# Kernel tuning notes

Measured on AMD Instinct MI355X. Metric: run time of the kernel, lower is better.

The kernel has to match this reference:

```python
import jax, jax.numpy as jnp
import numpy as np

N = 100_000   # nodes
E = 1_600_000 # edges (avg degree 16)
D = 128       # dim == dim_out
NEG_SLOPE = 0.2  # PyG GATConv default


def setup_inputs() -> dict:
    key = jax.random.key(0)
    ks = jax.random.split(key, 11)
    s = 1.0 / np.sqrt(D)
    return {
        "x": jax.random.normal(ks[0], (N, D), jnp.float32),
        "edge_index": jax.random.randint(ks[1], (2, E), 0, N, jnp.int32),
        "W1": jax.random.normal(ks[2], (D, D), jnp.float32) * s,
        "a_src1": jax.random.normal(ks[3], (D,), jnp.float32) * s,
        "a_dst1": jax.random.normal(ks[4], (D,), jnp.float32) * s,
        "b1": jnp.zeros((D,), jnp.float32),
        "W2": jax.random.normal(ks[5], (D, D), jnp.float32) * s,
        "a_src2": jax.random.normal(ks[6], (D,), jnp.float32) * s,
        "a_dst2": jax.random.normal(ks[7], (D,), jnp.float32) * s,
        "b2": jnp.zeros((D,), jnp.float32),
    }


def gat_conv(x, W, a_src, a_dst, b, src, dst, n):
    # PyG GATConv, heads=1: message flows src (j) -> dst (i)
    h = x @ W                              # [n, d]
    al_src = h @ a_src                     # per-node src attention logit
    al_dst = h @ a_dst                     # per-node dst attention logit
    e = jax.nn.leaky_relu(al_src[src] + al_dst[dst], NEG_SLOPE)  # [E']
    # softmax over incoming edges of each destination node (segment softmax)
    m = jax.ops.segment_max(e, dst, num_segments=n)
    e = jnp.exp(e - m[dst])
    z = jax.ops.segment_sum(e, dst, num_segments=n)
    alpha = e / z[dst]                     # [E']
    out = jax.ops.segment_sum(h[src] * alpha[:, None], dst, num_segments=n)
    return out + b


def reference(x, edge_index, W1, a_src1, a_dst1, b1, W2, a_src2, a_dst2, b2):
    n = x.shape[0]
    loop = jnp.arange(n, dtype=edge_index.dtype)
    src = jnp.concatenate([edge_index[0], loop])  # add_self_loops=True
    dst = jnp.concatenate([edge_index[1], loop])
    h = gat_conv(x, W1, a_src1, a_dst1, b1, src, dst, n)
    # self_loops=True -> residual=False; dropout in eval mode = identity
    return gat_conv(h, W2, a_src2, a_dst2, b2, src, dst, n)
```

## Files before the change

### kernel.cpp

```cpp
#include <hip/hip_runtime.h>
#include <hip/hip_bf16.h>
#include <math.h>

#define D 128
#define LRELU_SLOPE 0.2f
#define BSH 9
#define BSZ 512
#define BCAP 10240
#define SC_CHUNK 16384

typedef __attribute__((ext_vector_type(8))) short bf16x8;
typedef __attribute__((ext_vector_type(4))) float f32x4;

__device__ __forceinline__ float lrelu(float x){ return x > 0.f ? x : LRELU_SLOPE * x; }

__device__ __forceinline__ unsigned short bf16_rn(float x){
  unsigned int u = __float_as_uint(x);
  return (unsigned short)((u + 0x7FFFu + ((u >> 16) & 1u)) >> 16);
}
__device__ __forceinline__ float bf16_lo_f(unsigned int u){ return __uint_as_float(u << 16); }
__device__ __forceinline__ float bf16_hi_f(unsigned int u){ return __uint_as_float(u & 0xFFFF0000u); }

__device__ __forceinline__ unsigned int enc_f(float f){
  unsigned int u = __float_as_uint(f);
  return (u & 0x80000000u) ? ~u : (u | 0x80000000u);
}
__device__ __forceinline__ float dec_f(unsigned int e){
  return __uint_as_float((e & 0x80000000u) ? (e & 0x7FFFFFFFu) : ~e);
}

__global__ __launch_bounds__(1024) void bucket_scatter_kernel(const int* __restrict__ src,
    const int* __restrict__ dst, int E, int* __restrict__ bcur,
    unsigned int* __restrict__ ebuf, int nbuck){
  __shared__ int h[256];
  __shared__ int cb[256];
  int t = threadIdx.x;
  int base = blockIdx.x * SC_CHUNK;
  int end = base + SC_CHUNK; if (end > E) end = E;
  if (t < 256) h[t] = 0;
  __syncthreads();
  for (int e = base + t; e < end; e += 1024)
    atomicAdd(&h[dst[e] >> BSH], 1);
  __syncthreads();
  if (t < nbuck){
    cb[t] = h[t] ? atomicAdd(&bcur[t], h[t]) : 0;
    h[t] = 0;
  }
  __syncthreads();
  for (int e = base + t; e < end; e += 1024){
    int d = dst[e];
    int b = d >> BSH;
    int lpos = atomicAdd(&h[b], 1);
    ebuf[cb[b] + lpos] = ((unsigned int)src[e] << BSH) | (unsigned int)(d & (BSZ-1));
  }
}

__global__ __launch_bounds__(256) void bucket_csr_kernel(const unsigned int* __restrict__ ebuf,
    const int* __restrict__ bcur, int2* __restrict__ rowrange, int* __restrict__ colb,
    int n, int nbuck){
  __shared__ int c[512];
  __shared__ int ps[256];
  int b = blockIdx.x;
  int t = threadIdx.x;
  int base = b * BCAP;
  int end  = bcur[b];
  c[t] = 0; c[t+256] = 0;
  __syncthreads();
  for (int i = base + t; i < end; i += 256)
    atomicAdd(&c[ebuf[i] & (BSZ-1)], 1);
  __syncthreads();
  int a0 = c[2*t], a1 = c[2*t+1];
  int pair = a0 + a1;
  ps[t] = pair;
  __syncthreads();
  #pragma unroll
  for (int d = 1; d < 256; d <<= 1){
    int add = (t >= d) ? ps[t-d] : 0;
    __syncthreads();
    ps[t] += add;
    __syncthreads();
  }
  int excl = ps[t] - pair;
  __syncthreads();
  int lo = b << BSH;
  int g0 = lo + 2*t, g1 = g0 + 1;
  if (g0 < n) rowrange[g0] = make_int2(base + excl,      base + excl + a0);
  if (g1 < n) rowrange[g1] = make_int2(base + excl + a0, base + excl + a0 + a1);
  c[2*t]   = excl;
  c[2*t+1] = excl + a0;
  __syncthreads();
  for (int i = base + t; i < end; i += 256){
    unsigned int p = ebuf[i];
    int dlo = p & (BSZ-1);
    int pos = base + atomicAdd(&c[dlo], 1);
    colb[pos] = (int)(p >> BSH);
  }
}

__global__ __launch_bounds__(256) void wsplit_kernel(const float* __restrict__ W1,
    const float* __restrict__ W2,
    unsigned short* __restrict__ Whf1, unsigned short* __restrict__ Wlf1,
    unsigned short* __restrict__ Whf2, unsigned short* __restrict__ Wlf2){
  int b = blockIdx.x;
  const float* W = (b >= 64) ? W2 : W1;
  unsigned short* Whf = (b >= 64) ? Whf2 : Whf1;
  unsigned short* Wlf = (b >= 64) ? Wlf2 : Wlf1;
  int t = (b & 63)*256 + threadIdx.x;
  int k  = t >> 7;
  int nn = t & 127;
  float w = W[t];
  unsigned short h = bf16_rn(w);
  float whf = __uint_as_float(((unsigned int)h) << 16);
  unsigned short l = bf16_rn(w - whf);
  int kc = k >> 5, l4 = (k >> 3) & 3, e = k & 7;
  int cf = nn >> 4, l15 = nn & 15;
  int idx = ((kc*8 + cf)*64 + l4*16 + l15)*8 + e;
  Whf[idx] = h; Wlf[idx] = l;
}

__global__ __launch_bounds__(256) void wafrag_kernel(const float* __restrict__ W1,
    const float* __restrict__ W2,
    const float* __restrict__ as1, const float* __restrict__ ad1,
    const float* __restrict__ as2, const float* __restrict__ ad2,
    unsigned short* __restrict__ Whfx1, unsigned short* __restrict__ Wlfx1,
    unsigned short* __restrict__ Whfx2, unsigned short* __restrict__ Wlfx2,
    unsigned int* __restrict__ mx, int* __restrict__ bcur, int nbuck){
  __shared__ float wa[2][128];
  int layer = blockIdx.x;
  const float* W  = layer ? W2 : W1;
  const float* as = layer ? as2 : as1;
  const float* ad = layer ? ad2 : ad1;
  unsigned short* Whfx = layer ? Whfx2 : Whfx1;
  unsigned short* Wlfx = layer ? Wlfx2 : Wlfx1;
  int t = threadIdx.x;
  if (t < 2) mx[layer*2 + t] = 0u;
  if (layer == 0 && t < nbuck) bcur[t] = t * BCAP;

  int row = t & 127;
  const float* a = (t >> 7) ? ad : as;
  float s = 0.f;
  #pragma unroll 8
  for (int c = 0; c < 128; c += 4){
    float4 wv = *(const float4*)&W[row*128 + c];
    s += wv.x*a[c] + wv.y*a[c+1] + wv.z*a[c+2] + wv.w*a[c+3];
  }
  wa[t >> 7][row] = s;
  __syncthreads();

  int kc = t >> 6, lane = t & 63;
  int l15 = lane & 15, l4 = lane >> 4;
  unsigned short hh[8], ll[8];
  #pragma unroll
  for (int e = 0; e < 8; ++e){
    int k = (kc*4 + l4)*8 + e;
    float v = (l15 == 0) ? wa[0][k] : ((l15 == 1) ? wa[1][k] : 0.f);
    unsigned short h = bf16_rn(v);
    hh[e] = h;
    ll[e] = bf16_rn(v - __uint_as_float(((unsigned)h) << 16));
  }
  #pragma unroll
  for (int e = 0; e < 8; ++e){ Whfx[t*8 + e] = hh[e]; Wlfx[t*8 + e] = ll[e]; }
}

__global__ __launch_bounds__(256) void gemm_al_kernel(const float* __restrict__ X,
    const unsigned short* __restrict__ Whf, const unsigned short* __restrict__ Wlf,
    const unsigned short* __restrict__ Whfx, const unsigned short* __restrict__ Wlfx,
    unsigned short* __restrict__ Hb, float* __restrict__ ALs, float* __restrict__ ALd,
    unsigned int* __restrict__ mx, int n)
{
  __shared__ unsigned short Xh[128*128];
  __shared__ float redS[4], redD[4];
  int tid  = threadIdx.x;
  int lane = tid & 63;
  int wave = tid >> 6;
  int row0 = blockIdx.x * 128;
  int c4   = tid & 31;

  #pragma unroll 4
  for (int it = 0; it < 16; ++it){
    int f  = it*256 + tid;
    int r  = f >> 5;
    float4 v = make_float4(0.f,0.f,0.f,0.f);
    int gr = row0 + r;
    if (gr < n) v = ((const float4*)(X + (size_t)gr*D))[c4];
    unsigned short h0 = bf16_rn(v.x);
    unsigned short h1 = bf16_rn(v.y);
    unsigned short h2 = bf16_rn(v.z);
    unsigned short h3 = bf16_rn(v.w);
    int g   = (c4 >> 1) ^ (r & 7);
    int idx = r*128 + (g << 3) + ((c4 & 1) << 2);
    *(uint2*)&Xh[idx] = make_uint2((unsigned)h0 | ((unsigned)h1<<16),
                                   (unsigned)h2 | ((unsigned)h3<<16));
  }
  __syncthreads();

  int l15 = lane & 15;
  int l4  = lane >> 4;

  f32x4 acc[2][8];
  f32x4 acc2[2];
  #pragma unroll
  for (int rf = 0; rf < 2; ++rf){
    #pragma unroll
    for (int cf = 0; cf < 8; ++cf)
      acc[rf][cf] = (f32x4){0.f, 0.f, 0.f, 0.f};
    acc2[rf] = (f32x4){0.f, 0.f, 0.f, 0.f};
  }

  #pragma unroll
  for (int kc = 0; kc < 4; ++kc){
    int g = kc*4 + l4;
    bf16x8 ah[2];
    #pragma unroll
    for (int rf = 0; rf < 2; ++rf){
      int r   = wave*32 + rf*16 + l15;
      int idx = r*128 + ((g ^ (r & 7)) << 3);
      ah[rf] = *(const bf16x8*)&Xh[idx];
    }
    #pragma unroll
    for (int cf = 0; cf < 8; ++cf){
      int foff = ((kc*8 + cf) << 9) + (lane << 3);
      bf16x8 bh = *(const bf16x8*)&Whf[foff];
      bf16x8 bl = *(const bf16x8*)&Wlf[foff];
      #pragma unroll
      for (int rf = 0; rf < 2; ++rf){
        acc[rf][cf] = __builtin_amdgcn_mfma_f32_16x16x32_bf16(ah[rf], bh, acc[rf][cf], 0, 0, 0);
        acc[rf][cf] = __builtin_amdgcn_mfma_f32_16x16x32_bf16(ah[rf], bl, acc[rf][cf], 0, 0, 0);
      }
    }
    {
      int foffx = ((kc << 6) + lane) << 3;
      bf16x8 bhx = *(const bf16x8*)&Whfx[foffx];
      bf16x8 blx = *(const bf16x8*)&Wlfx[foffx];
      #pragma unroll
      for (int rf = 0; rf < 2; ++rf){
        acc2[rf] = __builtin_amdgcn_mfma_f32_16x16x32_bf16(ah[rf], bhx, acc2[rf], 0, 0, 0);
        acc2[rf] = __builtin_amdgcn_mfma_f32_16x16x32_bf16(ah[rf], blx, acc2[rf], 0, 0, 0);
      }
    }
  }

  float ms = -3e38f, md = -3e38f;
  #pragma unroll
  for (int rf = 0; rf < 2; ++rf){
    #pragma unroll
    for (int reg = 0; reg < 4; ++reg){
      int gr = row0 + wave*32 + rf*16 + l4*4 + reg;
      if (gr < n){
        unsigned int p0 = (unsigned)bf16_rn(acc[rf][0][reg]) | ((unsigned)bf16_rn(acc[rf][1][reg]) << 16);
        unsigned int p1 = (unsigned)bf16_rn(acc[rf][2][reg]) | ((unsigned)bf16_rn(acc[rf][3][reg]) << 16);
        unsigned int p2 = (unsigned)bf16_rn(acc[rf][4][reg]) | ((unsigned)bf16_rn(acc[rf][5][reg]) << 16);
        unsigned int p3 = (unsigned)bf16_rn(acc[rf][6][reg]) | ((unsigned)bf16_rn(acc[rf][7][reg]) << 16);
        ((uint4*)(Hb + (size_t)gr*D))[l15] = make_uint4(p0, p1, p2, p3);
        if (l15 == 0){      ALs[gr] = acc2[rf][reg]; ms = fmaxf(ms, acc2[rf][reg]); }
        else if (l15 == 1){ ALd[gr] = acc2[rf][reg]; md = fmaxf(md, acc2[rf][reg]); }
      }
    }
  }
  #pragma unroll
  for (int off = 32; off >= 1; off >>= 1){
    ms = fmaxf(ms, __shfl_xor(ms, off));
    md = fmaxf(md, __shfl_xor(md, off));
  }
  if (lane == 0){ redS[wave] = ms; redD[wave] = md; }
  __syncthreads();
  if (tid == 0){
    float a = fmaxf(fmaxf(redS[0], redS[1]), fmaxf(redS[2], redS[3]));
    float b = fmaxf(fmaxf(redD[0], redD[1]), fmaxf(redD[2], redD[3]));
    atomicMax(&mx[0], enc_f(a));
    atomicMax(&mx[1], enc_f(b));
  }
}

__global__ __launch_bounds__(256) void agg_kernel(const unsigned short* __restrict__ Hb,
    const float* __restrict__ ALs, const float* __restrict__ ALd,
    const unsigned int* __restrict__ mx,
    const int2* __restrict__ rowrange, const int* __restrict__ colb,
    const float* __restrict__ bias, float* __restrict__ out, int n)
{
  __shared__ unsigned int sArr[256];
  __shared__ float wArr[256];
  int gtid = blockIdx.x*blockDim.x + threadIdx.x;
  int node = gtid >> 6;
  int lane = threadIdx.x & 63;
  int wbase = threadIdx.x & 192;
  if (node >= n) return;

  float M = lrelu(dec_f(mx[0]) + dec_f(mx[1]));

  int2 rr = rowrange[node];
  int beg = rr.x, end = rr.y;
  float ald = ALd[node];
  float ws = __expf(lrelu(ALs[node] + ald) - M);

  const unsigned int* H2 = (const unsigned int*)Hb;
  unsigned int us = H2[(unsigned)(node*64 + lane)];
  float2 acc; acc.x = ws * bf16_lo_f(us); acc.y = ws * bf16_hi_f(us);
  float zl = 0.f;

  for (int c = beg; c < end; c += 64){
    int j = c + lane;
    bool valid = j < end;
    int s_l = valid ? colb[j] : 0;
    float w_l = valid ? __expf(lrelu(ALs[s_l] + ald) - M) : 0.f;
    zl += w_l;

    sArr[threadIdx.x] = (unsigned)s_l;
    wArr[threadIdx.x] = w_l;

    int cnt = end - c; if (cnt > 64) cnt = 64;
    int q = 0;
    for (; q + 8 <= cnt; q += 8){
      unsigned int ss[8]; float ww[8]; unsigned int u[8];
      #pragma unroll
      for (int p = 0; p < 8; ++p){ ss[p] = sArr[wbase + q + p]; ww[p] = wArr[wbase + q + p]; }
      #pragma unroll
      for (int p = 0; p < 8; ++p) u[p] = H2[(unsigned)(ss[p]*64u + lane)];
      #pragma unroll
      for (int p = 0; p < 8; ++p){
        acc.x += ww[p]*bf16_lo_f(u[p]);
        acc.y += ww[p]*bf16_hi_f(u[p]);
      }
    }
    for (; q < cnt; ++q){
      unsigned int u = H2[(unsigned)(sArr[wbase + q]*64u + lane)];
      float w = wArr[wbase + q];
      acc.x += w*bf16_lo_f(u); acc.y += w*bf16_hi_f(u);
    }
  }

  #pragma unroll
  for (int off = 32; off >= 1; off >>= 1) zl += __shfl_xor(zl, off);
  float zi = 1.f / (zl + ws);
  acc.x *= zi; acc.y *= zi;

  int q0 = (lane >> 4) + ((lane & 7) << 3);
  int q1 = q0 + 4;
  int hsel = (lane >> 3) & 1;
  float x0 = __shfl(acc.x, q0), y0 = __shfl(acc.y, q0);
  float x1 = __shfl(acc.x, q1), y1 = __shfl(acc.y, q1);
  float v0 = hsel ? y0 : x0;
  float v1 = hsel ? y1 : x1;

  float2 b2 = ((const float2*)bias)[lane];
  ((float2*)out)[(size_t)node*64 + lane] = make_float2(v0 + b2.x, v1 + b2.y);
}

extern "C" void kernel_launch(void* const* d_in, const int* in_sizes, int n_in,
                              void* d_out, int out_size, void* d_ws, size_t ws_size,
                              hipStream_t stream)
{
  const float* x   = (const float*)d_in[0];
  const int*   ei  = (const int*)  d_in[1];
  const float* W1  = (const float*)d_in[2];
  const float* as1 = (const float*)d_in[3];
  const float* ad1 = (const float*)d_in[4];
  const float* b1  = (const float*)d_in[5];
  const float* W2  = (const float*)d_in[6];
  const float* as2 = (const float*)d_in[7];
  const float* ad2 = (const float*)d_in[8];
  const float* b2  = (const float*)d_in[9];

  int n = in_sizes[0] / D;
  int E = in_sizes[1] / 2;
  const int* src = ei;
  const int* dst = ei + E;
  int nbuck = (n + BSZ - 1) >> BSH;

  char* base = (char*)d_ws;
  size_t off = 0;
  auto alloc = [&](size_t bytes) -> char* {
    char* p = base + off;
    off = (off + bytes + 255) & ~(size_t)255;
    return p;
  };
  unsigned short* hb = (unsigned short*)alloc((size_t)n*D*2);
  float* als    = (float*)alloc((size_t)n*4);
  float* ald    = (float*)alloc((size_t)n*4);
  int2* rowrange = (int2*)alloc((size_t)n*8);
  int* bcur     = (int*)alloc(256*4);
  unsigned int* mx = (unsigned int*)alloc(4*4);
  unsigned short* whf1 = (unsigned short*)alloc(16384*2);
  unsigned short* wlf1 = (unsigned short*)alloc(16384*2);
  unsigned short* whf2 = (unsigned short*)alloc(16384*2);
  unsigned short* wlf2 = (unsigned short*)alloc(16384*2);
  unsigned short* whfx1 = (unsigned short*)alloc(2048*2);
  unsigned short* wlfx1 = (unsigned short*)alloc(2048*2);
  unsigned short* whfx2 = (unsigned short*)alloc(2048*2);
  unsigned short* wlfx2 = (unsigned short*)alloc(2048*2);
  unsigned int* ebuf = (unsigned int*)alloc((size_t)nbuck*BCAP*4);
  int* colb = (int*)alloc((size_t)nbuck*BCAP*4);

  float* out = (float*)d_out;

  wsplit_kernel<<<128, 256, 0, stream>>>(W1, W2, whf1, wlf1, whf2, wlf2);
  wafrag_kernel<<<2, 256, 0, stream>>>(W1, W2, as1, ad1, as2, ad2,
                                       whfx1, wlfx1, whfx2, wlfx2, mx, bcur, nbuck);

  int sc_blocks = (E + SC_CHUNK - 1) / SC_CHUNK;
  bucket_scatter_kernel<<<sc_blocks, 1024, 0, stream>>>(src, dst, E, bcur, ebuf, nbuck);
  bucket_csr_kernel    <<<nbuck, 256, 0, stream>>>(ebuf, bcur, rowrange, colb, n, nbuck);

  int ntiles = (n + 127)/128;
  int aggblocks = (int)(((size_t)n*64 + 255)/256);

  gemm_al_kernel<<<ntiles, 256, 0, stream>>>(x,  whf1, wlf1, whfx1, wlfx1, hb, als, ald, mx,   n);
  agg_kernel    <<<aggblocks, 256, 0, stream>>>(hb, als, ald, mx,   rowrange, colb, b1, out, n);
  gemm_al_kernel<<<ntiles, 256, 0, stream>>>(out, whf2, wlf2, whfx2, wlfx2, hb, als, ald, mx+2, n);
  agg_kernel    <<<aggblocks, 256, 0, stream>>>(hb, als, ald, mx+2, rowrange, colb, b2, out, n);
}
```

Measured before the change: 287.9 us.

## Pass layer-1 output as permuted bf16 and halve GEMM row tile

```diff
diff --git a/kernel.cpp b/kernel.cpp
--- a/kernel.cpp
+++ b/kernel.cpp
@@ -28,6 +28,8 @@
 __device__ __forceinline__ float dec_f(unsigned int e){
   return __uint_as_float((e & 0x80000000u) ? (e & 0x7FFFFFFFu) : ~e);
 }
+
+__device__ __forceinline__ int colmap(int p){ return ((p & 7) << 4) + (p >> 3); }
 
 __global__ __launch_bounds__(1024) void bucket_scatter_kernel(const int* __restrict__ src,
     const int* __restrict__ dst, int E, int* __restrict__ bcur,
@@ -102,9 +104,10 @@
     unsigned short* __restrict__ Whf1, unsigned short* __restrict__ Wlf1,
     unsigned short* __restrict__ Whf2, unsigned short* __restrict__ Wlf2){
   int b = blockIdx.x;
-  const float* W = (b >= 64) ? W2 : W1;
-  unsigned short* Whf = (b >= 64) ? Whf2 : Whf1;
-  unsigned short* Wlf = (b >= 64) ? Wlf2 : Wlf1;
+  bool layer2 = (b >= 64);
+  const float* W = layer2 ? W2 : W1;
+  unsigned short* Whf = layer2 ? Whf2 : Whf1;
+  unsigned short* Wlf = layer2 ? Wlf2 : Wlf1;
   int t = (b & 63)*256 + threadIdx.x;
   int k  = t >> 7;
   int nn = t & 127;
@@ -112,7 +115,8 @@
   unsigned short h = bf16_rn(w);
   float whf = __uint_as_float(((unsigned int)h) << 16);
   unsigned short l = bf16_rn(w - whf);
-  int kc = k >> 5, l4 = (k >> 3) & 3, e = k & 7;
+  int ks = layer2 ? (((k & 15) << 3) + (k >> 4)) : k;
+  int kc = ks >> 5, l4 = (ks >> 3) & 3, e = ks & 7;
   int cf = nn >> 4, l15 = nn & 15;
   int idx = ((kc*8 + cf)*64 + l4*16 + l15)*8 + e;
   Whf[idx] = h; Wlf[idx] = l;
@@ -122,8 +126,10 @@
     const float* __restrict__ W2,
     const float* __restrict__ as1, const float* __restrict__ ad1,
     const float* __restrict__ as2, const float* __restrict__ ad2,
+    const float* __restrict__ b1,
     unsigned short* __restrict__ Whfx1, unsigned short* __restrict__ Wlfx1,
     unsigned short* __restrict__ Whfx2, unsigned short* __restrict__ Wlfx2,
+    float* __restrict__ bias_perm1,
     unsigned int* __restrict__ mx, int* __restrict__ bcur, int nbuck){
   __shared__ float wa[2][128];
   int layer = blockIdx.x;
@@ -135,6 +141,7 @@
   int t = threadIdx.x;
   if (t < 2) mx[layer*2 + t] = 0u;
   if (layer == 0 && t < nbuck) bcur[t] = t * BCAP;
+  if (layer == 0 && t < 128) bias_perm1[t] = b1[colmap(t)];
 
   int row = t & 127;
   const float* a = (t >> 7) ? ad : as;
@@ -152,7 +159,8 @@
   unsigned short hh[8], ll[8];
   #pragma unroll
   for (int e = 0; e < 8; ++e){
-    int k = (kc*4 + l4)*8 + e;
+    int ks = (kc*4 + l4)*8 + e;
+    int k  = layer ? colmap(ks) : ks;
     float v = (l15 == 0) ? wa[0][k] : ((l15 == 1) ? wa[1][k] : 0.f);
     unsigned short h = bf16_rn(v);
     hh[e] = h;
@@ -162,99 +170,97 @@
   for (int e = 0; e < 8; ++e){ Whfx[t*8 + e] = hh[e]; Wlfx[t*8 + e] = ll[e]; }
 }
 
-__global__ __launch_bounds__(256) void gemm_al_kernel(const float* __restrict__ X,
+template<bool BF16IN>
+__global__ __launch_bounds__(256) void gemm_al_kernel(const void* __restrict__ Xv,
     const unsigned short* __restrict__ Whf, const unsigned short* __restrict__ Wlf,
     const unsigned short* __restrict__ Whfx, const unsigned short* __restrict__ Wlfx,
     unsigned short* __restrict__ Hb, float* __restrict__ ALs, float* __restrict__ ALd,
     unsigned int* __restrict__ mx, int n)
 {
-  __shared__ unsigned short Xh[128*128];
+  __shared__ unsigned short Xh[64*128];
   __shared__ float redS[4], redD[4];
   int tid  = threadIdx.x;
   int lane = tid & 63;
   int wave = tid >> 6;
-  int row0 = blockIdx.x * 128;
-  int c4   = tid & 31;
-
-  #pragma unroll 4
-  for (int it = 0; it < 16; ++it){
-    int f  = it*256 + tid;
-    int r  = f >> 5;
-    float4 v = make_float4(0.f,0.f,0.f,0.f);
-    int gr = row0 + r;
-    if (gr < n) v = ((const float4*)(X + (size_t)gr*D))[c4];
-    unsigned short h0 = bf16_rn(v.x);
-    unsigned short h1 = bf16_rn(v.y);
-    unsigned short h2 = bf16_rn(v.z);
-    unsigned short h3 = bf16_rn(v.w);
-    int g   = (c4 >> 1) ^ (r & 7);
-    int idx = r*128 + (g << 3) + ((c4 & 1) << 2);
-    *(uint2*)&Xh[idx] = make_uint2((unsigned)h0 | ((unsigned)h1<<16),
-                                   (unsigned)h2 | ((unsigned)h3<<16));
+  int row0 = blockIdx.x * 64;
+
+  if constexpr (BF16IN){
+    const uint4* X4 = (const uint4*)Xv;
+    #pragma unroll
+    for (int it = 0; it < 4; ++it){
+      int f  = it*256 + tid;
+      int r  = f >> 4;
+      int pg = f & 15;
+      uint4 v = make_uint4(0u,0u,0u,0u);
+      int gr = row0 + r;
+      if (gr < n) v = X4[(size_t)gr*16 + pg];
+      *(uint4*)&Xh[r*128 + ((pg ^ (r & 7)) << 3)] = v;
+    }
+  } else {
+    const float* X = (const float*)Xv;
+    #pragma unroll 4
+    for (int it = 0; it < 8; ++it){
+      int f  = it*256 + tid;
+      int r  = f >> 5;
+      int c4 = f & 31;
+      float4 v = make_float4(0.f,0.f,0.f,0.f);
+      int gr = row0 + r;
+      if (gr < n) v = ((const float4*)(X + (size_t)gr*D))[c4];
+      unsigned short h0 = bf16_rn(v.x);
+      unsigned short h1 = bf16_rn(v.y);
+      unsigned short h2 = bf16_rn(v.z);
+      unsigned short h3 = bf16_rn(v.w);
+      int g   = (c4 >> 1) ^ (r & 7);
+      int idx = r*128 + (g << 3) + ((c4 & 1) << 2);
+      *(uint2*)&Xh[idx] = make_uint2((unsigned)h0 | ((unsigned)h1<<16),
+                                     (unsigned)h2 | ((unsigned)h3<<16));
+    }
   }
   __syncthreads();
 
   int l15 = lane & 15;
   int l4  = lane >> 4;
 
-  f32x4 acc[2][8];
-  f32x4 acc2[2];
-  #pragma unroll
-  for (int rf = 0; rf < 2; ++rf){
-    #pragma unroll
-    for (int cf = 0; cf < 8; ++cf)
-      acc[rf][cf] = (f32x4){0.f, 0.f, 0.f, 0.f};
-    acc2[rf] = (f32x4){0.f, 0.f, 0.f, 0.f};
-  }
+  f32x4 acc[8];
+  f32x4 acc2;
+  #pragma unroll
+  for (int cf = 0; cf < 8; ++cf) acc[cf] = (f32x4){0.f, 0.f, 0.f, 0.f};
+  acc2 = (f32x4){0.f, 0.f, 0.f, 0.f};
 
   #pragma unroll
   for (int kc = 0; kc < 4; ++kc){
     int g = kc*4 + l4;
-    bf16x8 ah[2];
-    #pragma unroll
-    for (int rf = 0; rf < 2; ++rf){
-      int r   = wave*32 + rf*16 + l15;
-      int idx = r*128 + ((g ^ (r & 7)) << 3);
-      ah[rf] = *(const bf16x8*)&Xh[idx];
-    }
+    int r = wave*16 + l15;
+    bf16x8 ah = *(const bf16x8*)&Xh[r*128 + ((g ^ (r & 7)) << 3)];
     #pragma unroll
     for (int cf = 0; cf < 8; ++cf){
       int foff = ((kc*8 + cf) << 9) + (lane << 3);
       bf16x8 bh = *(const bf16x8*)&Whf[foff];
       bf16x8 bl = *(const bf16x8*)&Wlf[foff];
-      #pragma unroll
-      for (int rf = 0; rf < 2; ++rf){
-        acc[rf][cf] = __builtin_amdgcn_mfma_f32_16x16x32_bf16(ah[rf], bh, acc[rf][cf], 0, 0, 0);
-        acc[rf][cf] = __builtin_amdgcn_mfma_f32_16x16x32_bf16(ah[rf], bl, acc[rf][cf], 0, 0, 0);
-      }
+      acc[cf] = __builtin_amdgcn_mfma_f32_16x16x32_bf16(ah, bh, acc[cf], 0, 0, 0);
+      acc[cf] = __builtin_amdgcn_mfma_f32_16x16x32_bf16(ah, bl, acc[cf], 0, 0, 0);
     }
     {
       int foffx = ((kc << 6) + lane) << 3;
       bf16x8 bhx = *(const bf16x8*)&Whfx[foffx];
       bf16x8 blx = *(const bf16x8*)&Wlfx[foffx];
-      #pragma unroll
-      for (int rf = 0; rf < 2; ++rf){
-        acc2[rf] = __builtin_amdgcn_mfma_f32_16x16x32_bf16(ah[rf], bhx, acc2[rf], 0, 0, 0);
-        acc2[rf] = __builtin_amdgcn_mfma_f32_16x16x32_bf16(ah[rf], blx, acc2[rf], 0, 0, 0);
-      }
+      acc2 = __builtin_amdgcn_mfma_f32_16x16x32_bf16(ah, bhx, acc2, 0, 0, 0);
+      acc2 = __builtin_amdgcn_mfma_f32_16x16x32_bf16(ah, blx, acc2, 0, 0, 0);
     }
   }
 
   float ms = -3e38f, md = -3e38f;
   #pragma unroll
-  for (int rf = 0; rf < 2; ++rf){
-    #pragma unroll
-    for (int reg = 0; reg < 4; ++reg){
-      int gr = row0 + wave*32 + rf*16 + l4*4 + reg;
-      if (gr < n){
-        unsigned int p0 = (unsigned)bf16_rn(acc[rf][0][reg]) | ((unsigned)bf16_rn(acc[rf][1][reg]) << 16);
-        unsigned int p1 = (unsigned)bf16_rn(acc[rf][2][reg]) | ((unsigned)bf16_rn(acc[rf][3][reg]) << 16);
-        unsigned int p2 = (unsigned)bf16_rn(acc[rf][4][reg]) | ((unsigned)bf16_rn(acc[rf][5][reg]) << 16);
-        unsigned int p3 = (unsigned)bf16_rn(acc[rf][6][reg]) | ((unsigned)bf16_rn(acc[rf][7][reg]) << 16);
-        ((uint4*)(Hb + (size_t)gr*D))[l15] = make_uint4(p0, p1, p2, p3);
-        if (l15 == 0){      ALs[gr] = acc2[rf][reg]; ms = fmaxf(ms, acc2[rf][reg]); }
-        else if (l15 == 1){ ALd[gr] = acc2[rf][reg]; md = fmaxf(md, acc2[rf][reg]); }
-      }
+  for (int reg = 0; reg < 4; ++reg){
+    int gr = row0 + wave*16 + l4*4 + reg;
+    if (gr < n){
+      unsigned int p0 = (unsigned)bf16_rn(acc[0][reg]) | ((unsigned)bf16_rn(acc[1][reg]) << 16);
+      unsigned int p1 = (unsigned)bf16_rn(acc[2][reg]) | ((unsigned)bf16_rn(acc[3][reg]) << 16);
+      unsigned int p2 = (unsigned)bf16_rn(acc[4][reg]) | ((unsigned)bf16_rn(acc[5][reg]) << 16);
+      unsigned int p3 = (unsigned)bf16_rn(acc[6][reg]) | ((unsigned)bf16_rn(acc[7][reg]) << 16);
+      ((uint4*)(Hb + (size_t)gr*D))[l15] = make_uint4(p0, p1, p2, p3);
+      if (l15 == 0){      ALs[gr] = acc2[reg]; ms = fmaxf(ms, acc2[reg]); }
+      else if (l15 == 1){ ALd[gr] = acc2[reg]; md = fmaxf(md, acc2[reg]); }
     }
   }
   #pragma unroll
@@ -272,11 +278,12 @@
   }
 }
 
+template<bool BF16OUT>
 __global__ __launch_bounds__(256) void agg_kernel(const unsigned short* __restrict__ Hb,
     const float* __restrict__ ALs, const float* __restrict__ ALd,
     const unsigned int* __restrict__ mx,
     const int2* __restrict__ rowrange, const int* __restrict__ colb,
-    const float* __restrict__ bias, float* __restrict__ out, int n)
+    const float* __restrict__ bias, void* __restrict__ outv, int n)
 {
   __shared__ unsigned int sArr[256];
   __shared__ float wArr[256];
@@ -334,16 +341,21 @@
   float zi = 1.f / (zl + ws);
   acc.x *= zi; acc.y *= zi;
 
-  int q0 = (lane >> 4) + ((lane & 7) << 3);
-  int q1 = q0 + 4;
-  int hsel = (lane >> 3) & 1;
-  float x0 = __shfl(acc.x, q0), y0 = __shfl(acc.y, q0);
-  float x1 = __shfl(acc.x, q1), y1 = __shfl(acc.y, q1);
-  float v0 = hsel ? y0 : x0;
-  float v1 = hsel ? y1 : x1;
-
-  float2 b2 = ((const float2*)bias)[lane];
-  ((float2*)out)[(size_t)node*64 + lane] = make_float2(v0 + b2.x, v1 + b2.y);
+  if constexpr (BF16OUT){
+    float2 bp = ((const float2*)bias)[lane];
+    unsigned int w = (unsigned)bf16_rn(acc.x + bp.x) | ((unsigned)bf16_rn(acc.y + bp.y) << 16);
+    ((unsigned int*)outv)[(unsigned)(node*64 + lane)] = w;
+  } else {
+    int q0 = (lane >> 4) + ((lane & 7) << 3);
+    int q1 = q0 + 4;
+    int hsel = (lane >> 3) & 1;
+    float x0 = __shfl(acc.x, q0), y0 = __shfl(acc.y, q0);
+    float x1 = __shfl(acc.x, q1), y1 = __shfl(acc.y, q1);
+    float v0 = hsel ? y0 : x0;
+    float v1 = hsel ? y1 : x1;
+    float2 b2 = ((const float2*)bias)[lane];
+    ((float2*)outv)[(size_t)node*64 + lane] = make_float2(v0 + b2.x, v1 + b2.y);
+  }
 }
 
 extern "C" void kernel_launch(void* const* d_in, const int* in_sizes, int n_in,
@@ -374,12 +386,14 @@
     off = (off + bytes + 255) & ~(size_t)255;
     return p;
   };
-  unsigned short* hb = (unsigned short*)alloc((size_t)n*D*2);
+  unsigned short* hb  = (unsigned short*)alloc((size_t)n*D*2);
+  unsigned short* hb2 = (unsigned short*)alloc((size_t)n*D*2);
   float* als    = (float*)alloc((size_t)n*4);
   float* ald    = (float*)alloc((size_t)n*4);
   int2* rowrange = (int2*)alloc((size_t)n*8);
   int* bcur     = (int*)alloc(256*4);
   unsigned int* mx = (unsigned int*)alloc(4*4);
+  float* bias_perm1 = (float*)alloc(128*4);
   unsigned short* whf1 = (unsigned short*)alloc(16384*2);
   unsigned short* wlf1 = (unsigned short*)alloc(16384*2);
   unsigned short* whf2 = (unsigned short*)alloc(16384*2);
@@ -394,18 +408,19 @@
   float* out = (float*)d_out;
 
   wsplit_kernel<<<128, 256, 0, stream>>>(W1, W2, whf1, wlf1, whf2, wlf2);
-  wafrag_kernel<<<2, 256, 0, stream>>>(W1, W2, as1, ad1, as2, ad2,
-                                       whfx1, wlfx1, whfx2, wlfx2, mx, bcur, nbuck);
+  wafrag_kernel<<<2, 256, 0, stream>>>(W1, W2, as1, ad1, as2, ad2, b1,
+                                       whfx1, wlfx1, whfx2, wlfx2,
+                                       bias_perm1, mx, bcur, nbuck);
 
   int sc_blocks = (E + SC_CHUNK - 1) / SC_CHUNK;
   bucket_scatter_kernel<<<sc_blocks, 1024, 0, stream>>>(src, dst, E, bcur, ebuf, nbuck);
   bucket_csr_kernel    <<<nbuck, 256, 0, stream>>>(ebuf, bcur, rowrange, colb, n, nbuck);
 
-  int ntiles = (n + 127)/128;
+  int ntiles = (n + 63)/64;
   int aggblocks = (int)(((size_t)n*64 + 255)/256);
 
-  gemm_al_kernel<<<ntiles, 256, 0, stream>>>(x,  whf1, wlf1, whfx1, wlfx1, hb, als, ald, mx,   n);
-  agg_kernel    <<<aggblocks, 256, 0, stream>>>(hb, als, ald, mx,   rowrange, colb, b1, out, n);
-  gemm_al_kernel<<<ntiles, 256, 0, stream>>>(out, whf2, wlf2, whfx2, wlfx2, hb, als, ald, mx+2, n);
-  agg_kernel    <<<aggblocks, 256, 0, stream>>>(hb, als, ald, mx+2, rowrange, colb, b2, out, n);
-}
+  gemm_al_kernel<false><<<ntiles, 256, 0, stream>>>(x,   whf1, wlf1, whfx1, wlfx1, hb, als, ald, mx,   n);
+  agg_kernel<true>     <<<aggblocks, 256, 0, stream>>>(hb, als, ald, mx,   rowrange, colb, bias_perm1, hb2, n);
+  gemm_al_kernel<true> <<<ntiles, 256, 0, stream>>>(hb2, whf2, wlf2, whfx2, wlfx2, hb, als, ald, mx+2, n);
+  agg_kernel<false>    <<<aggblocks, 256, 0, stream>>>(hb, als, ald, mx+2, rowrange, colb, b2, out, n);
+}
```

After: 310.7 us. 7.9% more time.
